# Kernel tuning notes

Hardware: AMD Instinct MI355X
Metric: run time of the kernel (lower is better)

Reference implementation:

```python
import jax, jax.numpy as jnp
import numpy as np

T, B = 512, 2048
IN, E, H = 12, 15, 20


def setup_inputs() -> dict:
    key = jax.random.key(0)
    ks = jax.random.split(key, 9)
    def rnd(k, shape, scale):
        return jax.random.normal(k, shape, dtype=jnp.float32) * scale
    return {
        "marker_detections": rnd(ks[0], (T, B, IN), 1.0),
        "W_emb": rnd(ks[1], (E, IN), 1.0 / np.sqrt(IN)),
        "b_emb": rnd(ks[2], (E,), 0.1),
        "W_ih": rnd(ks[3], (4 * H, E), 1.0 / np.sqrt(H)),
        "b_ih": rnd(ks[4], (4 * H,), 0.1),
        "W_hh": rnd(ks[5], (4 * H, H), 1.0 / np.sqrt(H)),
        "b_hh": rnd(ks[6], (4 * H,), 0.1),
        "W_out": rnd(ks[7], (3, H), 1.0 / np.sqrt(H)),
        "b_out": rnd(ks[8], (3,), 0.1),
    }


def _lstm(x_gates, W_hh, b_hh, hidden_dim):
    # x_gates: (T, B, 4H) precomputed input projections (PyTorch gate order i,f,g,o)
    Bsz = x_gates.shape[1]
    h0 = jnp.zeros((Bsz, hidden_dim), x_gates.dtype)
    c0 = jnp.zeros((Bsz, hidden_dim), x_gates.dtype)

    def step(carry, xg):
        h, c = carry
        gates = xg + h @ W_hh.T + b_hh  # (B, 4H)
        i, f, g, o = jnp.split(gates, 4, axis=-1)
        i = jax.nn.sigmoid(i)
        f = jax.nn.sigmoid(f)
        g = jnp.tanh(g)
        o = jax.nn.sigmoid(o)
        c = f * c + i * g
        h = o * jnp.tanh(c)
        return (h, c), h

    _, hs = jax.lax.scan(step, (h0, c0), x_gates)
    return hs  # (T, B, H)


def reference(marker_detections, W_emb, b_emb, W_ih, b_ih, W_hh, b_hh, W_out, b_out):
    # embeddings: (T, B, E)
    emb = marker_detections @ W_emb.T + b_emb
    # precompute input-to-gate projections for all timesteps: (T, B, 4H)
    x_gates = emb @ W_ih.T + b_ih
    hs = _lstm(x_gates, W_hh, b_hh, H)  # (T, B, H)
    pos_space = hs @ W_out.T + b_out  # (T, B, 3)
    return pos_space
```

## Files before the change

kernel.cpp:

```cpp
#include <hip/hip_runtime.h>

#define T_STEPS 512
#define BATCH   2048
#define IN_F    12
#define E_F     15
#define H_F     20
#define G4      80
#define TC      32
#define NCHUNK  (T_STEPS / TC)

typedef float v2f __attribute__((ext_vector_type(2)));

#define OFF_MD   0
#define OFF_HH   768
#define OFF_WC   (768 + 1536)
#define OFF_BC   (OFF_WC + 960)
#define OFF_WO   (OFF_BC + 80)
#define OFF_RAW  (OFF_WO + 80)
#define RAW_WEMB 0
#define RAW_WIH  180
#define RAW_BEMB 1380
#define RAW_BIH  1395
#define RAW_BHH  1475
#define SMEM_FLOATS (OFF_RAW + 1555)

__device__ __forceinline__ float fsig(float x) {
    float e = __builtin_amdgcn_exp2f(x * -1.442695040888963f);
    return __builtin_amdgcn_rcpf(1.0f + e);
}
__device__ __forceinline__ float ftanh(float x) {
    float e = __builtin_amdgcn_exp2f(x * -2.885390081777927f);
    return fmaf(2.0f, __builtin_amdgcn_rcpf(1.0f + e), -1.0f);
}
__device__ __forceinline__ v2f pkfma(v2f a, v2f b, v2f c) {
    return __builtin_elementwise_fma(a, b, c);
}

__global__ void __launch_bounds__(64)
__attribute__((amdgpu_waves_per_eu(1, 1)))
lstm_tracker_kernel(
    const float* __restrict__ md,
    const float* __restrict__ W_emb, const float* __restrict__ b_emb,
    const float* __restrict__ W_ih,  const float* __restrict__ b_ih,
    const float* __restrict__ W_hh,  const float* __restrict__ b_hh,
    const float* __restrict__ W_out, const float* __restrict__ b_out,
    float* __restrict__ out)
{
    __shared__ __align__(16) float smem[SMEM_FLOATS];
    const int lane = threadIdx.x;
    const int bl   = lane >> 5;
    const int j    = lane & 31;
    const int jj   = (j < H_F) ? j : 0;
    const size_t bbase = (size_t)blockIdx.x * 2;

    float* raw = smem + OFF_RAW;
    for (int i = lane; i < E_F * IN_F; i += 64) raw[RAW_WEMB + i] = W_emb[i];
    for (int i = lane; i < G4 * E_F;  i += 64) raw[RAW_WIH  + i] = W_ih[i];
    if (lane < E_F) raw[RAW_BEMB + lane] = b_emb[lane];
    for (int g = lane; g < G4; g += 64) raw[RAW_BIH + g] = b_ih[g];
    for (int g = lane; g < G4; g += 64) raw[RAW_BHH + g] = b_hh[g];
    for (int i = lane; i < 3 * H_F; i += 64) {
        int r = i / H_F, k = i - r * H_F;
        smem[OFF_WO + r * 24 + k] = W_out[i];
    }
    if (lane < 3) smem[OFF_WO + 72 + lane] = b_out[lane];

    for (int idx = lane; idx < G4 * IN_F; idx += 64) {
        int g = idx / IN_F, c = idx - g * IN_F;
        float s = 0.f;
        #pragma unroll
        for (int e = 0; e < E_F; ++e)
            s += raw[RAW_WIH + g * E_F + e] * raw[RAW_WEMB + e * IN_F + c];
        smem[OFF_WC + idx] = s;
    }
    for (int g = lane; g < G4; g += 64) {
        float s = raw[RAW_BIH + g] + raw[RAW_BHH + g];
        #pragma unroll
        for (int e = 0; e < E_F; ++e)
            s += raw[RAW_WIH + g * E_F + e] * raw[RAW_BEMB + e];
        smem[OFF_BC + g] = s;
    }

    v2f wcI[6], wcF[6], wcG[6], wcO[6];
    #pragma unroll
    for (int k = 0; k < 6; ++k) {
        wcI[k] = *(const v2f*)(smem + OFF_WC + (jj           ) * IN_F + 2 * k);
        wcF[k] = *(const v2f*)(smem + OFF_WC + (jj +     H_F ) * IN_F + 2 * k);
        wcG[k] = *(const v2f*)(smem + OFF_WC + (jj + 2 * H_F ) * IN_F + 2 * k);
        wcO[k] = *(const v2f*)(smem + OFF_WC + (jj + 3 * H_F ) * IN_F + 2 * k);
    }
    const float bcI = smem[OFF_BC + jj];
    const float bcF = smem[OFF_BC + jj + H_F];
    const float bcG = smem[OFF_BC + jj + 2 * H_F];
    const float bcO = smem[OFF_BC + jj + 3 * H_F];

    v2f whI[10], whF[10], whG[10], whO[10];
    #pragma unroll
    for (int k = 0; k < 10; ++k) {
        whI[k] = *(const v2f*)(W_hh + (jj           ) * H_F + 2 * k);
        whF[k] = *(const v2f*)(W_hh + (jj +     H_F ) * H_F + 2 * k);
        whG[k] = *(const v2f*)(W_hh + (jj + 2 * H_F ) * H_F + 2 * k);
        whO[k] = *(const v2f*)(W_hh + (jj + 3 * H_F ) * H_F + 2 * k);
    }

    v2f h2[10];
    #pragma unroll
    for (int k = 0; k < 10; ++k) h2[k] = (v2f){0.f, 0.f};
    float cc = 0.f;

    #pragma unroll 1
    for (int ch = 0; ch < NCHUNK; ++ch) {
        for (int idx = lane; idx < TC * 6; idx += 64) {
            int tt = idx / 6, w = idx - tt * 6;
            const float* src = md + ((size_t)(ch * TC + tt) * BATCH + bbase) * IN_F + w * 4;
            *(float4*)(smem + OFF_MD + tt * 24 + w * 4) = *(const float4*)src;
        }

        const float4* mr0 = (const float4*)(smem + OFF_MD + bl * IN_F);
        float4 m0 = mr0[0], m1 = mr0[1], m2 = mr0[2];

        #pragma unroll 1
        for (int tt = 0; tt < TC; ++tt) {
            v2f mm0 = {m0.x, m0.y}, mm1 = {m0.z, m0.w}, mm2 = {m1.x, m1.y};
            v2f mm3 = {m1.z, m1.w}, mm4 = {m2.x, m2.y}, mm5 = {m2.z, m2.w};
            v2f aI = pkfma(wcI[0], mm0, pkfma(wcI[1], mm1, pkfma(wcI[2], mm2,
                     pkfma(wcI[3], mm3, pkfma(wcI[4], mm4, pkfma(wcI[5], mm5, (v2f){bcI, 0.f}))))));
            v2f aF = pkfma(wcF[0], mm0, pkfma(wcF[1], mm1, pkfma(wcF[2], mm2,
                     pkfma(wcF[3], mm3, pkfma(wcF[4], mm4, pkfma(wcF[5], mm5, (v2f){bcF, 0.f}))))));
            v2f aG = pkfma(wcG[0], mm0, pkfma(wcG[1], mm1, pkfma(wcG[2], mm2,
                     pkfma(wcG[3], mm3, pkfma(wcG[4], mm4, pkfma(wcG[5], mm5, (v2f){bcG, 0.f}))))));
            v2f aO = pkfma(wcO[0], mm0, pkfma(wcO[1], mm1, pkfma(wcO[2], mm2,
                     pkfma(wcO[3], mm3, pkfma(wcO[4], mm4, pkfma(wcO[5], mm5, (v2f){bcO, 0.f}))))));

            if (tt + 1 < TC) {
                const float4* mn = (const float4*)(smem + OFF_MD + (tt + 1) * 24 + bl * IN_F);
                m0 = mn[0]; m1 = mn[1]; m2 = mn[2];
            }

            v2f rIa = pkfma(whI[0], h2[0], pkfma(whI[1], h2[1], pkfma(whI[2], h2[2],
                      pkfma(whI[3], h2[3], whI[4] * h2[4]))));
            v2f rIb = pkfma(whI[5], h2[5], pkfma(whI[6], h2[6], pkfma(whI[7], h2[7],
                      pkfma(whI[8], h2[8], whI[9] * h2[9]))));
            v2f rFa = pkfma(whF[0], h2[0], pkfma(whF[1], h2[1], pkfma(whF[2], h2[2],
                      pkfma(whF[3], h2[3], whF[4] * h2[4]))));
            v2f rFb = pkfma(whF[5], h2[5], pkfma(whF[6], h2[6], pkfma(whF[7], h2[7],
                      pkfma(whF[8], h2[8], whF[9] * h2[9]))));
            v2f rGa = pkfma(whG[0], h2[0], pkfma(whG[1], h2[1], pkfma(whG[2], h2[2],
                      pkfma(whG[3], h2[3], whG[4] * h2[4]))));
            v2f rGb = pkfma(whG[5], h2[5], pkfma(whG[6], h2[6], pkfma(whG[7], h2[7],
                      pkfma(whG[8], h2[8], whG[9] * h2[9]))));
            v2f rOa = pkfma(whO[0], h2[0], pkfma(whO[1], h2[1], pkfma(whO[2], h2[2],
                      pkfma(whO[3], h2[3], whO[4] * h2[4]))));
            v2f rOb = pkfma(whO[5], h2[5], pkfma(whO[6], h2[6], pkfma(whO[7], h2[7],
                      pkfma(whO[8], h2[8], whO[9] * h2[9]))));

            v2f sI = aI + rIa + rIb;
            v2f sF = aF + rFa + rFb;
            v2f sG = aG + rGa + rGb;
            v2f sO = aO + rOa + rOb;
            float ai = sI.x + sI.y;
            float af = sF.x + sF.y;
            float ag = sG.x + sG.y;
            float ao = sO.x + sO.y;

            float gi = fsig(ai);
            float gf = fsig(af);
            float gt = ftanh(ag);
            float go = fsig(ao);
            cc = fmaf(gf, cc, gi * gt);
            float hown = go * ftanh(cc);

            float* hslot = smem + OFF_HH + tt * 48 + bl * 24;
            if (j < H_F) hslot[jj] = hown;
            const float4* hr = (const float4*)hslot;
            float4 h0 = hr[0], h1 = hr[1], hx = hr[2], h3 = hr[3], h4 = hr[4];
            h2[0] = (v2f){h0.x, h0.y}; h2[1] = (v2f){h0.z, h0.w};
            h2[2] = (v2f){h1.x, h1.y}; h2[3] = (v2f){h1.z, h1.w};
            h2[4] = (v2f){hx.x, hx.y}; h2[5] = (v2f){hx.z, hx.w};
            h2[6] = (v2f){h3.x, h3.y}; h2[7] = (v2f){h3.z, h3.w};
            h2[8] = (v2f){h4.x, h4.y}; h2[9] = (v2f){h4.z, h4.w};
        }

        for (int idx = lane; idx < TC * 6; idx += 64) {
            int tt = idx / 6, rem = idx - tt * 6;
            int bb = rem / 3, r = rem - bb * 3;
            const float4* hp = (const float4*)(smem + OFF_HH + tt * 48 + bb * 24);
            const float4* wp = (const float4*)(smem + OFF_WO + r * 24);
            float s = smem[OFF_WO + 72 + r];
            #pragma unroll
            for (int k = 0; k < 5; ++k) {
                float4 hv = hp[k], wv = wp[k];
                s += hv.x * wv.x + hv.y * wv.y + hv.z * wv.z + hv.w * wv.w;
            }
            out[((size_t)(ch * TC + tt) * BATCH + bbase + bb) * 3 + r] = s;
        }
    }
}

extern "C" void kernel_launch(void* const* d_in, const int* in_sizes, int n_in,
                              void* d_out, int out_size, void* d_ws, size_t ws_size,
                              hipStream_t stream) {
    const float* md    = (const float*)d_in[0];
    const float* W_emb = (const float*)d_in[1];
    const float* b_emb = (const float*)d_in[2];
    const float* W_ih  = (const float*)d_in[3];
    const float* b_ih  = (const float*)d_in[4];
    const float* W_hh  = (const float*)d_in[5];
    const float* b_hh  = (const float*)d_in[6];
    const float* W_out = (const float*)d_in[7];
    const float* b_out = (const float*)d_in[8];
    float* out = (float*)d_out;

    hipLaunchKernelGGL(lstm_tracker_kernel, dim3(BATCH / 2), dim3(64), 0, stream,
                       md, W_emb, b_emb, W_ih, b_ih, W_hh, b_hh, W_out, b_out, out);
}
```

Before: 281.8 us.

## Precompute per-chunk input gate projections in shared memory before recurrence

Instead of each lane computing its four gates' input projections inside the serial time loop, the whole wave first computes all gate pre-activations for the chunk into a shared buffer (gate-interleaved), then the recurrence reads one float4 per step. W_hh is staged through LDS with inline ds_read_b64 asm, and the hidden-state slot stride is tightened. This moves the input-projection FMAs off the serial dependency chain and uses all 64 lanes (including the idle ones) for it. The cost is extra LDS traffic and a larger shared footprint.

```diff
diff --git a/kernel.cpp b/kernel.cpp
--- a/kernel.cpp
+++ b/kernel.cpp
@@ -13,16 +13,18 @@
 
 #define OFF_MD   0
 #define OFF_HH   768
-#define OFF_WC   (768 + 1536)
-#define OFF_BC   (OFF_WC + 960)
-#define OFF_WO   (OFF_BC + 80)
-#define OFF_RAW  (OFF_WO + 80)
-#define RAW_WEMB 0
-#define RAW_WIH  180
-#define RAW_BEMB 1380
-#define RAW_BIH  1395
-#define RAW_BHH  1475
-#define SMEM_FLOATS (OFF_RAW + 1555)
+#define OFF_XG   2048
+#define OFF_WC   7168
+#define OFF_BC   8128
+#define OFF_WO   8208
+#define OFF_WHH  8288
+#define SMEM_FLOATS 9888
+
+#define RAW_WEMB (OFF_XG + 0)
+#define RAW_WIH  (OFF_XG + 180)
+#define RAW_BEMB (OFF_XG + 1380)
+#define RAW_BIH  (OFF_XG + 1395)
+#define RAW_BHH  (OFF_XG + 1475)
 
 __device__ __forceinline__ float fsig(float x) {
     float e = __builtin_amdgcn_exp2f(x * -1.442695040888963f);
@@ -35,6 +37,18 @@
 __device__ __forceinline__ v2f pkfma(v2f a, v2f b, v2f c) {
     return __builtin_elementwise_fma(a, b, c);
 }
+
+#define LD10(arr, breg) \
+    asm volatile("ds_read_b64 %0, %1 offset:0"  : "=v"(arr[0]) : "v"(breg) : "memory"); \
+    asm volatile("ds_read_b64 %0, %1 offset:8"  : "=v"(arr[1]) : "v"(breg) : "memory"); \
+    asm volatile("ds_read_b64 %0, %1 offset:16" : "=v"(arr[2]) : "v"(breg) : "memory"); \
+    asm volatile("ds_read_b64 %0, %1 offset:24" : "=v"(arr[3]) : "v"(breg) : "memory"); \
+    asm volatile("ds_read_b64 %0, %1 offset:32" : "=v"(arr[4]) : "v"(breg) : "memory"); \
+    asm volatile("ds_read_b64 %0, %1 offset:40" : "=v"(arr[5]) : "v"(breg) : "memory"); \
+    asm volatile("ds_read_b64 %0, %1 offset:48" : "=v"(arr[6]) : "v"(breg) : "memory"); \
+    asm volatile("ds_read_b64 %0, %1 offset:56" : "=v"(arr[7]) : "v"(breg) : "memory"); \
+    asm volatile("ds_read_b64 %0, %1 offset:64" : "=v"(arr[8]) : "v"(breg) : "memory"); \
+    asm volatile("ds_read_b64 %0, %1 offset:72" : "=v"(arr[9]) : "v"(breg) : "memory");
 
 __global__ void __launch_bounds__(64)
 __attribute__((amdgpu_waves_per_eu(1, 1)))
@@ -53,54 +67,43 @@
     const int jj   = (j < H_F) ? j : 0;
     const size_t bbase = (size_t)blockIdx.x * 2;
 
-    float* raw = smem + OFF_RAW;
-    for (int i = lane; i < E_F * IN_F; i += 64) raw[RAW_WEMB + i] = W_emb[i];
-    for (int i = lane; i < G4 * E_F;  i += 64) raw[RAW_WIH  + i] = W_ih[i];
-    if (lane < E_F) raw[RAW_BEMB + lane] = b_emb[lane];
-    for (int g = lane; g < G4; g += 64) raw[RAW_BIH + g] = b_ih[g];
-    for (int g = lane; g < G4; g += 64) raw[RAW_BHH + g] = b_hh[g];
+    for (int i = lane; i < E_F * IN_F; i += 64) smem[RAW_WEMB + i] = W_emb[i];
+    for (int i = lane; i < G4 * E_F;  i += 64) smem[RAW_WIH  + i] = W_ih[i];
+    if (lane < E_F) smem[RAW_BEMB + lane] = b_emb[lane];
+    for (int g = lane; g < G4; g += 64) smem[RAW_BIH + g] = b_ih[g];
+    for (int g = lane; g < G4; g += 64) smem[RAW_BHH + g] = b_hh[g];
     for (int i = lane; i < 3 * H_F; i += 64) {
         int r = i / H_F, k = i - r * H_F;
         smem[OFF_WO + r * 24 + k] = W_out[i];
     }
     if (lane < 3) smem[OFF_WO + 72 + lane] = b_out[lane];
+    for (int i = lane; i < G4 * H_F; i += 64) smem[OFF_WHH + i] = W_hh[i];
 
     for (int idx = lane; idx < G4 * IN_F; idx += 64) {
         int g = idx / IN_F, c = idx - g * IN_F;
         float s = 0.f;
         #pragma unroll
         for (int e = 0; e < E_F; ++e)
-            s += raw[RAW_WIH + g * E_F + e] * raw[RAW_WEMB + e * IN_F + c];
+            s += smem[RAW_WIH + g * E_F + e] * smem[RAW_WEMB + e * IN_F + c];
         smem[OFF_WC + idx] = s;
     }
     for (int g = lane; g < G4; g += 64) {
-        float s = raw[RAW_BIH + g] + raw[RAW_BHH + g];
+        float s = smem[RAW_BIH + g] + smem[RAW_BHH + g];
         #pragma unroll
         for (int e = 0; e < E_F; ++e)
-            s += raw[RAW_WIH + g * E_F + e] * raw[RAW_BEMB + e];
+            s += smem[RAW_WIH + g * E_F + e] * smem[RAW_BEMB + e];
         smem[OFF_BC + g] = s;
     }
 
-    v2f wcI[6], wcF[6], wcG[6], wcO[6];
-    #pragma unroll
-    for (int k = 0; k < 6; ++k) {
-        wcI[k] = *(const v2f*)(smem + OFF_WC + (jj           ) * IN_F + 2 * k);
-        wcF[k] = *(const v2f*)(smem + OFF_WC + (jj +     H_F ) * IN_F + 2 * k);
-        wcG[k] = *(const v2f*)(smem + OFF_WC + (jj + 2 * H_F ) * IN_F + 2 * k);
-        wcO[k] = *(const v2f*)(smem + OFF_WC + (jj + 3 * H_F ) * IN_F + 2 * k);
-    }
-    const float bcI = smem[OFF_BC + jj];
-    const float bcF = smem[OFF_BC + jj + H_F];
-    const float bcG = smem[OFF_BC + jj + 2 * H_F];
-    const float bcO = smem[OFF_BC + jj + 3 * H_F];
-
     v2f whI[10], whF[10], whG[10], whO[10];
-    #pragma unroll
-    for (int k = 0; k < 10; ++k) {
-        whI[k] = *(const v2f*)(W_hh + (jj           ) * H_F + 2 * k);
-        whF[k] = *(const v2f*)(W_hh + (jj +     H_F ) * H_F + 2 * k);
-        whG[k] = *(const v2f*)(W_hh + (jj + 2 * H_F ) * H_F + 2 * k);
-        whO[k] = *(const v2f*)(W_hh + (jj + 3 * H_F ) * H_F + 2 * k);
+    {
+        const int bI = OFF_WHH * 4 + jj * 80;
+        const int bF = bI + 1600;
+        const int bG = bI + 3200;
+        const int bO = bI + 4800;
+        LD10(whI, bI); LD10(whF, bF); LD10(whG, bG); LD10(whO, bO);
+        asm volatile("s_waitcnt lgkmcnt(0)" ::: "memory");
+        __builtin_amdgcn_sched_barrier(0);
     }
 
     v2f h2[10];
@@ -116,52 +119,41 @@
             *(float4*)(smem + OFF_MD + tt * 24 + w * 4) = *(const float4*)src;
         }
 
-        const float4* mr0 = (const float4*)(smem + OFF_MD + bl * IN_F);
-        float4 m0 = mr0[0], m1 = mr0[1], m2 = mr0[2];
-
+        for (int base = 0; base < TC * 160; base += 64) {
+            int idx = base + lane;
+            int tt = idx / 160, r = idx - tt * 160;
+            int bb = (r >= G4) ? 1 : 0;
+            int gi = r - bb * G4;
+            int sel = gi / H_F, ju = gi - sel * H_F;
+            const float4* m4 = (const float4*)(smem + OFF_MD + tt * 24 + bb * IN_F);
+            const float4* w4 = (const float4*)(smem + OFF_WC + gi * IN_F);
+            float4 m0 = m4[0], m1 = m4[1], m2 = m4[2];
+            float4 q0 = w4[0], q1 = w4[1], q2 = w4[2];
+            float s = smem[OFF_BC + gi];
+            s += m0.x*q0.x + m0.y*q0.y + m0.z*q0.z + m0.w*q0.w
+               + m1.x*q1.x + m1.y*q1.y + m1.z*q1.z + m1.w*q1.w
+               + m2.x*q2.x + m2.y*q2.y + m2.z*q2.z + m2.w*q2.w;
+            smem[OFF_XG + (tt * 2 + bb) * G4 + ju * 4 + sel] = s;
+        }
+
+        float4 xv = *(const float4*)(smem + OFF_XG + bl * G4 + jj * 4);
         #pragma unroll 1
         for (int tt = 0; tt < TC; ++tt) {
-            v2f mm0 = {m0.x, m0.y}, mm1 = {m0.z, m0.w}, mm2 = {m1.x, m1.y};
-            v2f mm3 = {m1.z, m1.w}, mm4 = {m2.x, m2.y}, mm5 = {m2.z, m2.w};
-            v2f aI = pkfma(wcI[0], mm0, pkfma(wcI[1], mm1, pkfma(wcI[2], mm2,
-                     pkfma(wcI[3], mm3, pkfma(wcI[4], mm4, pkfma(wcI[5], mm5, (v2f){bcI, 0.f}))))));
-            v2f aF = pkfma(wcF[0], mm0, pkfma(wcF[1], mm1, pkfma(wcF[2], mm2,
-                     pkfma(wcF[3], mm3, pkfma(wcF[4], mm4, pkfma(wcF[5], mm5, (v2f){bcF, 0.f}))))));
-            v2f aG = pkfma(wcG[0], mm0, pkfma(wcG[1], mm1, pkfma(wcG[2], mm2,
-                     pkfma(wcG[3], mm3, pkfma(wcG[4], mm4, pkfma(wcG[5], mm5, (v2f){bcG, 0.f}))))));
-            v2f aO = pkfma(wcO[0], mm0, pkfma(wcO[1], mm1, pkfma(wcO[2], mm2,
-                     pkfma(wcO[3], mm3, pkfma(wcO[4], mm4, pkfma(wcO[5], mm5, (v2f){bcO, 0.f}))))));
-
-            if (tt + 1 < TC) {
-                const float4* mn = (const float4*)(smem + OFF_MD + (tt + 1) * 24 + bl * IN_F);
-                m0 = mn[0]; m1 = mn[1]; m2 = mn[2];
+            const int tn = (tt + 1 < TC) ? tt + 1 : tt;
+            float4 xnext = *(const float4*)(smem + OFF_XG + (tn * 2 + bl) * G4 + jj * 4);
+
+            v2f aI = {xv.x, 0.f}, aF = {xv.y, 0.f}, aG = {xv.z, 0.f}, aO = {xv.w, 0.f};
+            #pragma unroll
+            for (int k = 0; k < 10; ++k) {
+                aI = pkfma(whI[k], h2[k], aI);
+                aF = pkfma(whF[k], h2[k], aF);
+                aG = pkfma(whG[k], h2[k], aG);
+                aO = pkfma(whO[k], h2[k], aO);
             }
-
-            v2f rIa = pkfma(whI[0], h2[0], pkfma(whI[1], h2[1], pkfma(whI[2], h2[2],
-                      pkfma(whI[3], h2[3], whI[4] * h2[4]))));
-            v2f rIb = pkfma(whI[5], h2[5], pkfma(whI[6], h2[6], pkfma(whI[7], h2[7],
-                      pkfma(whI[8], h2[8], whI[9] * h2[9]))));
-            v2f rFa = pkfma(whF[0], h2[0], pkfma(whF[1], h2[1], pkfma(whF[2], h2[2],
-                      pkfma(whF[3], h2[3], whF[4] * h2[4]))));
-            v2f rFb = pkfma(whF[5], h2[5], pkfma(whF[6], h2[6], pkfma(whF[7], h2[7],
-                      pkfma(whF[8], h2[8], whF[9] * h2[9]))));
-            v2f rGa = pkfma(whG[0], h2[0], pkfma(whG[1], h2[1], pkfma(whG[2], h2[2],
-                      pkfma(whG[3], h2[3], whG[4] * h2[4]))));
-            v2f rGb = pkfma(whG[5], h2[5], pkfma(whG[6], h2[6], pkfma(whG[7], h2[7],
-                      pkfma(whG[8], h2[8], whG[9] * h2[9]))));
-            v2f rOa = pkfma(whO[0], h2[0], pkfma(whO[1], h2[1], pkfma(whO[2], h2[2],
-                      pkfma(whO[3], h2[3], whO[4] * h2[4]))));
-            v2f rOb = pkfma(whO[5], h2[5], pkfma(whO[6], h2[6], pkfma(whO[7], h2[7],
-                      pkfma(whO[8], h2[8], whO[9] * h2[9]))));
-
-            v2f sI = aI + rIa + rIb;
-            v2f sF = aF + rFa + rFb;
-            v2f sG = aG + rGa + rGb;
-            v2f sO = aO + rOa + rOb;
-            float ai = sI.x + sI.y;
-            float af = sF.x + sF.y;
-            float ag = sG.x + sG.y;
-            float ao = sO.x + sO.y;
+            float ai = aI.x + aI.y;
+            float af = aF.x + aF.y;
+            float ag = aG.x + aG.y;
+            float ao = aO.x + aO.y;
 
             float gi = fsig(ai);
             float gf = fsig(af);
@@ -170,8 +162,8 @@
             cc = fmaf(gf, cc, gi * gt);
             float hown = go * ftanh(cc);
 
-            float* hslot = smem + OFF_HH + tt * 48 + bl * 24;
-            if (j < H_F) hslot[jj] = hown;
+            float* hslot = smem + OFF_HH + tt * 40 + bl * 20;
+            if (j < H_F) hslot[j] = hown;
             const float4* hr = (const float4*)hslot;
             float4 h0 = hr[0], h1 = hr[1], hx = hr[2], h3 = hr[3], h4 = hr[4];
             h2[0] = (v2f){h0.x, h0.y}; h2[1] = (v2f){h0.z, h0.w};
@@ -179,12 +171,14 @@
             h2[4] = (v2f){hx.x, hx.y}; h2[5] = (v2f){hx.z, hx.w};
             h2[6] = (v2f){h3.x, h3.y}; h2[7] = (v2f){h3.z, h3.w};
             h2[8] = (v2f){h4.x, h4.y}; h2[9] = (v2f){h4.z, h4.w};
+
+            xv = xnext;
         }
 
         for (int idx = lane; idx < TC * 6; idx += 64) {
             int tt = idx / 6, rem = idx - tt * 6;
             int bb = rem / 3, r = rem - bb * 3;
-            const float4* hp = (const float4*)(smem + OFF_HH + tt * 48 + bb * 24);
+            const float4* hp = (const float4*)(smem + OFF_HH + tt * 40 + bb * 20);
             const float4* wp = (const float4*)(smem + OFF_WO + r * 24);
             float s = smem[OFF_WO + 72 + r];
             #pragma unroll
```

Result: slower. 420.2 us (+49.1%).
